# Kernel tuning notes

Measured on AMD Instinct MI355X. Metric: run time of the kernel, lower is better.

Reference implementation:

```python
import jax, jax.numpy as jnp
import numpy as np

RADIUS = 0.2
MAX_SAMPLES = 64


def setup_inputs() -> dict:
    key = jax.random.key(0)
    k1, k2 = jax.random.split(key)
    B, N, M = 4, 16384, 2048
    pcs = jax.random.uniform(k1, (B, N, 3), dtype=jnp.float32)
    # centroids sampled from the same unit cube (as if FPS-sampled from pcs)
    centroids = jax.random.uniform(k2, (B, M, 3), dtype=jnp.float32)
    return {"pcs": pcs, "centroids": centroids}


def reference(pcs, centroids):
    """Ball point query: for each centroid, the indices of up to MAX_SAMPLES
    points within RADIUS, in ascending point-index order; remaining slots are
    padded with the first found index (PointNet++ convention). Returns
    int64 group_idx of shape [B, M, MAX_SAMPLES]."""
    B, N, _ = pcs.shape
    r2 = jnp.float32(RADIUS * RADIUS)
    # squared distances [B, M, N] via expansion (avoids materializing diffs [B,M,N,3])
    p2 = jnp.sum(pcs * pcs, axis=-1)              # [B, N]
    c2 = jnp.sum(centroids * centroids, axis=-1)  # [B, M]
    cross = jnp.einsum("bmd,bnd->bmn", centroids, pcs)  # [B, M, N]
    d2 = c2[:, :, None] + p2[:, None, :] - 2.0 * cross
    # encode valid point indices so that top_k picks the SMALLEST indices first:
    # key = N - idx for in-ball points (large key <-> small idx), 0 for out-of-ball
    idx_keys = (N - jnp.arange(N, dtype=jnp.int32))[None, None, :]  # [1,1,N]
    keys = jnp.where(d2 <= r2, idx_keys, 0)  # [B, M, N] int32
    top_vals, _ = jax.lax.top_k(keys, MAX_SAMPLES)  # [B, M, K]
    idx = N - top_vals  # invalid slots (key==0) become N
    first = idx[..., :1]
    group_idx = jnp.where(idx == N, first, idx)
    return group_idx.astype(jnp.int64)
```

## Files before the change

kernel.cpp:

```cpp
#include <hip/hip_runtime.h>

#define N_PTS 16384
#define M_CENT 2048
#define MAXS 64
#define WPB 4
#define CHUNK 256

__global__ __launch_bounds__(256) void ball_query_kernel(
    const float* __restrict__ pcs,
    const float* __restrict__ cent,
    int* __restrict__ out)
{
#pragma clang fp contract(off)
    __shared__ int slots[WPB][MAXS];

    const int lane = threadIdx.x & 63;
    const int wid  = threadIdx.x >> 6;
    const int cg   = blockIdx.x * WPB + wid;
    const int b    = cg >> 11;

    const float* cp = cent + (size_t)cg * 3;
    const float cx = cp[0], cy = cp[1], cz = cp[2];
    float c2 = cx * cx;
    c2 += cy * cy;
    c2 += cz * cz;
    const float r2 = 0.04f;

    const float* pbase = pcs + (size_t)b * N_PTS * 3;

    const float4* q = (const float4*)(pbase) + (size_t)lane * 3;

    int count = 0;
    int base = 0;
    float4 a = q[0], bb = q[1], cc = q[2];

    while (true) {
        const int nbase = base + CHUNK;
        const bool have_next = nbase < N_PTS;
        float4 na, nb, nc;
        if (have_next) {
            const float4* qn = q + (size_t)(nbase >> 4) * 16 - ((size_t)(base >> 4) * 16);
            const float4* qq = (const float4*)(pbase) + (size_t)(nbase / 4) * 3 + (size_t)lane * 3;
            na = qq[0]; nb = qq[1]; nc = qq[2];
            (void)qn;
        }

        float p2, cr, d2;
        p2 = a.x * a.x;  p2 += a.y * a.y;  p2 += a.z * a.z;
        cr = cx * a.x;   cr += cy * a.y;   cr += cz * a.z;
        d2 = (c2 + p2) - 2.0f * cr;
        const bool h0 = d2 <= r2;

        p2 = a.w * a.w;  p2 += bb.x * bb.x;  p2 += bb.y * bb.y;
        cr = cx * a.w;   cr += cy * bb.x;    cr += cz * bb.y;
        d2 = (c2 + p2) - 2.0f * cr;
        const bool h1 = d2 <= r2;

        p2 = bb.z * bb.z;  p2 += bb.w * bb.w;  p2 += cc.x * cc.x;
        cr = cx * bb.z;    cr += cy * bb.w;    cr += cz * cc.x;
        d2 = (c2 + p2) - 2.0f * cr;
        const bool h2 = d2 <= r2;

        p2 = cc.y * cc.y;  p2 += cc.z * cc.z;  p2 += cc.w * cc.w;
        cr = cx * cc.y;    cr += cy * cc.z;    cr += cz * cc.w;
        d2 = (c2 + p2) - 2.0f * cr;
        const bool h3 = d2 <= r2;

        const unsigned long long m0 = __ballot(h0);
        const unsigned long long m1 = __ballot(h1);
        const unsigned long long m2 = __ballot(h2);
        const unsigned long long m3 = __ballot(h3);
        const unsigned long long pre = (1ull << lane) - 1ull;

        const int below = (int)__popcll(m0 & pre) + (int)__popcll(m1 & pre)
                        + (int)__popcll(m2 & pre) + (int)__popcll(m3 & pre);
        const int r0 = count + below;
        const int r1 = r0 + (int)((m0 >> lane) & 1ull);
        const int r2i = r1 + (int)((m1 >> lane) & 1ull);
        const int r3 = r2i + (int)((m2 >> lane) & 1ull);

        const int pidx = base + 4 * lane;
        if (h0 && r0  < MAXS) slots[wid][r0]  = pidx;
        if (h1 && r1  < MAXS) slots[wid][r1]  = pidx + 1;
        if (h2 && r2i < MAXS) slots[wid][r2i] = pidx + 2;
        if (h3 && r3  < MAXS) slots[wid][r3]  = pidx + 3;

        count += (int)__popcll(m0) + (int)__popcll(m1)
               + (int)__popcll(m2) + (int)__popcll(m3);

        if (count >= MAXS || !have_next) break;
        a = na; bb = nb; cc = nc; base = nbase;
    }

    __syncthreads();

    const int cnt = count < MAXS ? count : MAXS;
    int val;
    if (cnt == 0) {
        val = N_PTS;
    } else {
        val = (lane < cnt) ? slots[wid][lane] : slots[wid][0];
    }
    out[((size_t)cg << 6) + lane] = val;
}

extern "C" void kernel_launch(void* const* d_in, const int* in_sizes, int n_in,
                              void* d_out, int out_size, void* d_ws, size_t ws_size,
                              hipStream_t stream) {
    const float* pcs  = (const float*)d_in[0];
    const float* cent = (const float*)d_in[1];
    int* out = (int*)d_out;

    const int B = in_sizes[0] / (N_PTS * 3);
    const int total_centroids = B * M_CENT;
    const int grid = total_centroids / WPB;

    ball_query_kernel<<<grid, 256, 0, stream>>>(pcs, cent, out);
}
```

Baseline: 86.21 us.

## Split each centroid's point scan across four waves with block-level prefix counts

Each block now handles one centroid instead of four. The four waves scan interleaved 256-point chunks, so each iteration covers 1024 points, and a per-iteration __syncthreads plus shared wave counts produce a cross-wave prefix offset for ordered slot writes. This shortens the serial per-centroid scan, which matters because the radius is small and many centroids must scan far before finding 64 hits. In exchange it adds a block barrier every iteration, wastes work on the wave that finishes past the early-exit point, and launches four times as many blocks.

```diff
diff --git a/kernel.cpp b/kernel.cpp
--- a/kernel.cpp
+++ b/kernel.cpp
@@ -3,8 +3,8 @@
 #define N_PTS 16384
 #define M_CENT 2048
 #define MAXS 64
-#define WPB 4
-#define CHUNK 256
+#define NWAVE 4
+#define NITER 16
 
 __global__ __launch_bounds__(256) void ball_query_kernel(
     const float* __restrict__ pcs,
@@ -12,11 +12,12 @@
     int* __restrict__ out)
 {
 #pragma clang fp contract(off)
-    __shared__ int slots[WPB][MAXS];
+    __shared__ int slots[MAXS];
+    __shared__ int wavecnt[2][NWAVE];
 
     const int lane = threadIdx.x & 63;
     const int wid  = threadIdx.x >> 6;
-    const int cg   = blockIdx.x * WPB + wid;
+    const int cg   = blockIdx.x;
     const int b    = cg >> 11;
 
     const float* cp = cent + (size_t)cg * 3;
@@ -27,22 +28,20 @@
     const float r2 = 0.04f;
 
     const float* pbase = pcs + (size_t)b * N_PTS * 3;
-
-    const float4* q = (const float4*)(pbase) + (size_t)lane * 3;
+    const float4* pq = (const float4*)pbase;
+    const int toff = wid * 64 + lane;
 
     int count = 0;
-    int base = 0;
-    float4 a = q[0], bb = q[1], cc = q[2];
+    size_t qi = (size_t)3 * toff;
+    float4 a = pq[qi], bb = pq[qi + 1], cc = pq[qi + 2];
 
+    int iter = 0;
     while (true) {
-        const int nbase = base + CHUNK;
-        const bool have_next = nbase < N_PTS;
+        const bool have_next = (iter + 1) < NITER;
         float4 na, nb, nc;
         if (have_next) {
-            const float4* qn = q + (size_t)(nbase >> 4) * 16 - ((size_t)(base >> 4) * 16);
-            const float4* qq = (const float4*)(pbase) + (size_t)(nbase / 4) * 3 + (size_t)lane * 3;
-            na = qq[0]; nb = qq[1]; nc = qq[2];
-            (void)qn;
+            const size_t nq = (size_t)3 * ((iter + 1) * 256 + toff);
+            na = pq[nq]; nb = pq[nq + 1]; nc = pq[nq + 2];
         }
 
         float p2, cr, d2;
@@ -72,36 +71,50 @@
         const unsigned long long m3 = __ballot(h3);
         const unsigned long long pre = (1ull << lane) - 1ull;
 
+        const int mycnt = (int)__popcll(m0) + (int)__popcll(m1)
+                        + (int)__popcll(m2) + (int)__popcll(m3);
+        if (lane == 0) wavecnt[iter & 1][wid] = mycnt;
+        __syncthreads();
+
+        int prew = 0, tot = 0;
+#pragma unroll
+        for (int w = 0; w < NWAVE; ++w) {
+            const int c = wavecnt[iter & 1][w];
+            tot += c;
+            if (w < wid) prew += c;
+        }
+
         const int below = (int)__popcll(m0 & pre) + (int)__popcll(m1 & pre)
                         + (int)__popcll(m2 & pre) + (int)__popcll(m3 & pre);
-        const int r0 = count + below;
-        const int r1 = r0 + (int)((m0 >> lane) & 1ull);
+        const int r0 = count + prew + below;
+        const int r1 = r0  + (int)((m0 >> lane) & 1ull);
         const int r2i = r1 + (int)((m1 >> lane) & 1ull);
         const int r3 = r2i + (int)((m2 >> lane) & 1ull);
 
-        const int pidx = base + 4 * lane;
-        if (h0 && r0  < MAXS) slots[wid][r0]  = pidx;
-        if (h1 && r1  < MAXS) slots[wid][r1]  = pidx + 1;
-        if (h2 && r2i < MAXS) slots[wid][r2i] = pidx + 2;
-        if (h3 && r3  < MAXS) slots[wid][r3]  = pidx + 3;
+        const int pidx = 4 * (iter * 256 + toff);
+        if (h0 && r0  < MAXS) slots[r0]  = pidx;
+        if (h1 && r1  < MAXS) slots[r1]  = pidx + 1;
+        if (h2 && r2i < MAXS) slots[r2i] = pidx + 2;
+        if (h3 && r3  < MAXS) slots[r3]  = pidx + 3;
 
-        count += (int)__popcll(m0) + (int)__popcll(m1)
-               + (int)__popcll(m2) + (int)__popcll(m3);
-
-        if (count >= MAXS || !have_next) break;
-        a = na; bb = nb; cc = nc; base = nbase;
+        count += tot;
+        ++iter;
+        if (count >= MAXS || iter >= NITER) break;
+        a = na; bb = nb; cc = nc;
     }
 
     __syncthreads();
 
-    const int cnt = count < MAXS ? count : MAXS;
-    int val;
-    if (cnt == 0) {
-        val = N_PTS;
-    } else {
-        val = (lane < cnt) ? slots[wid][lane] : slots[wid][0];
+    if (wid == 0) {
+        const int cnt = count < MAXS ? count : MAXS;
+        int val;
+        if (cnt == 0) {
+            val = N_PTS;
+        } else {
+            val = (lane < cnt) ? slots[lane] : slots[0];
+        }
+        out[((size_t)cg << 6) + lane] = val;
     }
-    out[((size_t)cg << 6) + lane] = val;
 }
 
 extern "C" void kernel_launch(void* const* d_in, const int* in_sizes, int n_in,
@@ -112,8 +125,7 @@
     int* out = (int*)d_out;
 
     const int B = in_sizes[0] / (N_PTS * 3);
-    const int total_centroids = B * M_CENT;
-    const int grid = total_centroids / WPB;
+    const int grid = B * M_CENT;
 
     ball_query_kernel<<<grid, 256, 0, stream>>>(pcs, cent, out);
 }
```

Result: faster. 76.84 us (-10.9%).
